# Performance work log

Hardware: AMD Instinct MI355X
Metric: run time of the kernel (lower is better)

## Reference

```python
import jax, jax.numpy as jnp
import numpy as np

N = 2060          # drug-graph nodes (m_drug_d_num)
F_OUT = 901       # out_feats, forced by Linear(901*2, ...)
M = 901 + (N - 1183)  # 1778 fused node rows
E = N * 64
N_TRAIN, N_TEST = 100000, 30000
EPS = 1e-5


def setup_inputs() -> dict:
    key = jax.random.key(0)
    ks = jax.random.split(key, 30)
    f32 = jnp.float32
    inp = {
        'x_feat': jax.random.normal(ks[0], (N, N), f32),
        'mirna_feat': jax.random.normal(ks[1], (M, F_OUT), f32),
        'Wg': jax.random.normal(ks[2], (N, F_OUT), f32) * 0.02,
        'att_src': jax.random.normal(ks[3], (F_OUT,), f32) * 0.05,
        'att_dst': jax.random.normal(ks[4], (F_OUT,), f32) * 0.05,
        'gat_b': jnp.zeros((F_OUT,), f32),
        'lw1': jax.random.normal(ks[5], (1, 2), f32) * 0.5,
        'lb1': jnp.zeros((1,), f32),
        'lw2': jax.random.normal(ks[6], (2, 1), f32) * 0.5,
        'lb2': jnp.zeros((2,), f32),
        'gw1': jax.random.normal(ks[7], (1, 2), f32) * 0.5,
        'gb1': jnp.zeros((1,), f32),
        'gw2': jax.random.normal(ks[8], (2, 1), f32) * 0.5,
        'gb2': jnp.zeros((2,), f32),
        'W1': jax.random.normal(ks[9], (2 * F_OUT, 1024), f32) * 0.02,
        'b1': jnp.zeros((1024,), f32),
        'W2': jax.random.normal(ks[10], (1024, 512), f32) * 0.03,
        'b2': jnp.zeros((512,), f32),
        'W3': jax.random.normal(ks[11], (512, 64), f32) * 0.04,
        'b3': jnp.zeros((64,), f32),
        'W4': jax.random.normal(ks[12], (64, 1), f32) * 0.1,
        'b4': jnp.zeros((1,), f32),
        'edge_index': jax.random.randint(ks[13], (2, E), 0, N, jnp.int32),
        'train_sample': jax.random.randint(ks[14], (N_TRAIN, 2), 0, M, jnp.int32),
        'test_sample': jax.random.randint(ks[15], (N_TEST, 2), 0, M, jnp.int32),
    }
    return inp


def _bn(x, axes):
    # BatchNorm in train mode (fresh module: gamma=1, beta=0, biased batch var)
    mu = x.mean(axes, keepdims=True)
    var = x.var(axes, keepdims=True)
    return (x - mu) * jax.lax.rsqrt(var + EPS)


def _gat(x, Wg, att_src, att_dst, gat_b, edge_index):
    # single-head PyG-style GATConv with self loops, negative_slope=0.2
    h = x @ Wg                                         # [N, F]
    loop = jnp.arange(N, dtype=edge_index.dtype)
    src = jnp.concatenate([edge_index[0], loop])
    dst = jnp.concatenate([edge_index[1], loop])
    a_s = h @ att_src                                  # [N]
    a_d = h @ att_dst
    e = jax.nn.leaky_relu(a_s[src] + a_d[dst], 0.2)    # per-edge logits
    emax = jax.ops.segment_max(e, dst, num_segments=N)
    ex = jnp.exp(e - emax[dst])
    denom = jax.ops.segment_sum(ex, dst, num_segments=N)
    alpha = ex / denom[dst]
    out = jax.ops.segment_sum(alpha[:, None] * h[src], dst, num_segments=N) + gat_b
    return jax.nn.relu(out)                            # F.relu in MGL (MGC relu is idempotent)


def _forward(x_feat, mirna_feat, Wg, att_src, att_dst, gat_b,
             lw1, lb1, lw2, lb2, gw1, gb1, gw2, gb2,
             W1, b1, W2, b2, W3, b3, W4, b4,
             edge_index, train_sample, test_sample):
    g = _gat(x_feat, Wg, att_src, att_dst, gat_b, edge_index)      # [N, 901]
    drug_view = jnp.concatenate([g[:901], g[1183:]], axis=0)       # [M, 901]
    x = jnp.stack([drug_view, mirna_feat], axis=1)                 # [M, 2, 901]  (B=M, C=2, H=1 dropped, W=901)

    # MS_CAM (channels=2, r=2), BN in train mode
    xl = jnp.einsum('mcw,oc->mow', x, lw1) + lb1[None, :, None]    # [M, 1, 901]
    xl = jax.nn.relu(_bn(xl, (0, 2)))
    xl = jnp.einsum('mcw,oc->mow', xl, lw2) + lb2[None, :, None]   # [M, 2, 901]
    xl = _bn(xl, (0, 2))

    gp = x.mean(axis=2)                                            # [M, 2] global avg pool
    xg = gp @ gw1.T + gb1                                          # [M, 1]
    xg = jax.nn.relu(_bn(xg, (0,)))
    xg = xg @ gw2.T + gb2                                          # [M, 2]
    xg = _bn(xg, (0,))

    wei = jax.nn.sigmoid(xl + xg[:, :, None])
    x = x * wei                                                    # [M, 2, 901]
    fused = (x[:, 0, :] + x[:, 1, :]) * 0.5                        # [M, 901]

    def score(pairs):
        emb = jnp.concatenate([fused[pairs[:, 0]], fused[pairs[:, 1]]], axis=1)  # [B, 1802]
        h = emb @ W1 + b1
        h = h @ W2 + b2
        h = h @ W3 + b3
        return jax.nn.sigmoid(h @ W4 + b4)

    return score(train_sample), score(test_sample)


def reference(x_feat, mirna_feat, Wg, att_src, att_dst, gat_b,
              lw1, lb1, lw2, lb2, gw1, gb1, gw2, gb2,
              W1, b1, W2, b2, W3, b3, W4, b4,
              edge_index, train_sample, test_sample):
    return _forward(x_feat, mirna_feat, Wg, att_src, att_dst, gat_b,
                    lw1, lb1, lw2, lb2, gw1, gb1, gw2, gb2,
                    W1, b1, W2, b2, W3, b3, W4, b4,
                    edge_index, train_sample, test_sample)
```

## Files before the change

kernel.cpp:

```cpp
#include <hip/hip_runtime.h>

typedef unsigned short u16;
typedef unsigned int   u32;

#define NN   2060
#define FF   901
#define HP   904
#define MM   1778
#define EE   131840
#define ETOT 133900
#define NTR  100000
#define NOUT 130000
#define MP   2112
#define KP   2080
#define NP   960
#define EPSV 1e-5f
#define NTOT 1601978.0

typedef __attribute__((ext_vector_type(4))) float f32x4;
typedef __attribute__((ext_vector_type(8))) short bf16x8;

#define GLL16(g,l) __builtin_amdgcn_global_load_lds( \
    (const __attribute__((address_space(1))) u32*)(g), \
    (__attribute__((address_space(3))) u32*)(l), 16, 0, 0)

__device__ __forceinline__ float bf2f(u16 u){ return __uint_as_float(((u32)u)<<16); }
__device__ __forceinline__ u16 f2bf(float f){
  u32 b = __float_as_uint(f);
  return (u16)((b + 0x7fffu + ((b>>16)&1u)) >> 16);
}
__device__ __forceinline__ float ldf(const void* p, size_t i, int bf){
  return bf ? bf2f(((const u16*)p)[i]) : ((const float*)p)[i];
}
__device__ __forceinline__ u16 ldb(const void* p, size_t i, int bf){
  return bf ? ((const u16*)p)[i] : f2bf(((const float*)p)[i]);
}
__device__ __forceinline__ float waveSum(float v){
  #pragma unroll
  for (int o = 32; o; o >>= 1) v += __shfl_down(v, o);
  return v;
}
__device__ __forceinline__ int waveSumI(int v){
  #pragma unroll
  for (int o = 32; o; o >>= 1) v += __shfl_down(v, o);
  return v;
}
__device__ __forceinline__ int flagWave(const u32* __restrict__ x){
  int l = threadIdx.x & 63;
  u32 w0 = x[l], w1 = x[l + 64];
  int big = (((w0 >> 7)  & 0xFFu) >= 0xC0u) + (((w0 >> 23) & 0xFFu) >= 0xC0u)
          + (((w1 >> 7)  & 0xFFu) >= 0xC0u) + (((w1 >> 23) & 0xFFu) >= 0xC0u);
  big = waveSumI(big);
  return (__shfl(big, 0) >= 8) ? 0 : 1;
}

__global__ __launch_bounds__(256) void pad_k(const void* __restrict__ X, const void* __restrict__ Wg,
                                             u16* __restrict__ Ap, u16* __restrict__ BT, int* bfp){
  __shared__ u16 tt[32][33];
  int bf = flagWave((const u32*)X);
  int bx = blockIdx.x, by = blockIdx.y, tid = threadIdx.x;
  if (bx == 0 && by == 0 && tid == 0) *bfp = bf;
  if (by < MP){
    int col = bx * 256 + tid, row = by;
    if (col >= KP) return;
    u16 v = 0;
    if (row < NN && col < NN) v = ldb(X, (size_t)row * NN + col, bf);
    Ap[(size_t)row * KP + col] = v;
  } else {
    if (bx) return;
    int t = by - MP;
    int kb = (t % 65) * 32, nb = (t / 65) * 32;
    int tx = tid & 31, ty = tid >> 5;
    #pragma unroll
    for (int i = 0; i < 4; ++i){
      int k = kb + ty + 8*i, n = nb + tx;
      u16 v = 0;
      if (k < NN && n < FF) v = ldb(Wg, (size_t)k * FF + n, bf);
      tt[ty + 8*i][tx] = v;
    }
    __syncthreads();
    #pragma unroll
    for (int i = 0; i < 4; ++i){
      int n = nb + ty + 8*i, k = kb + tx;
      if (n < NP && k < KP) BT[(size_t)n * KP + k] = tt[tx][ty + 8*i];
    }
  }
}

__global__ __launch_bounds__(256) void gemm_k(const u16* __restrict__ A, const u16* __restrict__ BT,
                                              u16* __restrict__ h){
  __shared__ __align__(16) u16 sA[64*32];
  __shared__ __align__(16) u16 sB[64*32];
  int bm = blockIdx.x * 64, bn = blockIdx.y * 64;
  int tid = threadIdx.x, lane = tid & 63, wave = tid >> 6;
  int wm = (wave >> 1) * 32, wn = (wave & 1) * 32;
  f32x4 acc[2][2] = {};
  int srow = tid >> 2;
  int schunk = (tid & 3) ^ ((tid >> 3) & 3);
  const u16* gA = A  + (size_t)(bm + srow) * KP + schunk * 8;
  const u16* gB = BT + (size_t)(bn + srow) * KP + schunk * 8;
  u16* lA = sA + wave * 512;
  u16* lB = sB + wave * 512;
  int fr = lane & 15, quad = lane >> 4;
  int qs = quad ^ ((fr >> 1) & 3);
  const u16* pa0 = &sA[(wm      + fr) * 32 + qs * 8];
  const u16* pa1 = &sA[(wm + 16 + fr) * 32 + qs * 8];
  const u16* pb0 = &sB[(wn      + fr) * 32 + qs * 8];
  const u16* pb1 = &sB[(wn + 16 + fr) * 32 + qs * 8];
  const int KIT = KP / 32;
  for (int kt = 0; kt < KIT; ++kt){
    __syncthreads();
    GLL16(gA + kt * 32, lA);
    GLL16(gB + kt * 32, lB);
    __syncthreads();
    bf16x8 a0 = *(const bf16x8*)pa0;
    bf16x8 a1 = *(const bf16x8*)pa1;
    bf16x8 b0 = *(const bf16x8*)pb0;
    bf16x8 b1 = *(const bf16x8*)pb1;
    acc[0][0] = __builtin_amdgcn_mfma_f32_16x16x32_bf16(a0, b0, acc[0][0], 0,0,0);
    acc[0][1] = __builtin_amdgcn_mfma_f32_16x16x32_bf16(a0, b1, acc[0][1], 0,0,0);
    acc[1][0] = __builtin_amdgcn_mfma_f32_16x16x32_bf16(a1, b0, acc[1][0], 0,0,0);
    acc[1][1] = __builtin_amdgcn_mfma_f32_16x16x32_bf16(a1, b1, acc[1][1], 0,0,0);
  }
  #pragma unroll
  for (int im = 0; im < 2; ++im)
    #pragma unroll
    for (int in = 0; in < 2; ++in)
      #pragma unroll
      for (int i = 0; i < 4; ++i){
        int row = bm + wm + im*16 + quad*4 + i;
        int col = bn + wn + in*16 + fr;
        if (row < NN && col < FF) h[(size_t)row * HP + col] = f2bf(acc[im][in][i]);
      }
}

__global__ __launch_bounds__(64) void asd_k(const u16* __restrict__ h, const void* att_s, const void* att_d,
                                            float* a_s, float* a_d, const int* bfp){
  int bf = *bfp;
  int n = blockIdx.x, tid = threadIdx.x;
  float ss = 0, sd = 0;
  for (int f = tid; f < FF; f += 64){
    float hv = bf2f(h[(size_t)n * HP + f]);
    ss += hv * ldf(att_s, f, bf);
    sd += hv * ldf(att_d, f, bf);
  }
  ss = waveSum(ss); sd = waveSum(sd);
  if (tid == 0){ a_s[n] = ss; a_d[n] = sd; }
}

__global__ __launch_bounds__(256) void edge1_k(const int* __restrict__ ei, const float* __restrict__ a_s,
                                               const float* __restrict__ a_d, float* __restrict__ e_val,
                                               u32* __restrict__ emax, int* __restrict__ counts){
  int e = blockIdx.x * 256 + threadIdx.x;
  if (e >= ETOT) return;
  int src, dst;
  if (e < EE){ src = ei[e]; dst = ei[EE + e]; } else { src = dst = e - EE; }
  float x = a_s[src] + a_d[dst];
  float ev = x > 0.f ? x : 0.2f * x;
  e_val[e] = ev;
  u32 bits = __float_as_uint(ev);
  u32 enc = (bits & 0x80000000u) ? ~bits : (bits | 0x80000000u);
  atomicMax(&emax[dst], enc);
  atomicAdd(&counts[dst], 1);
}

__global__ __launch_bounds__(256) void scan_k(const int* __restrict__ counts, int* __restrict__ offs){
  __shared__ int part[256];
  int tid = threadIdx.x;
  const int CH = (NN + 255) / 256;
  int base = tid * CH, s = 0;
  for (int i = 0; i < CH; ++i){ int idx = base + i; if (idx < NN) s += counts[idx]; }
  part[tid] = s;
  __syncthreads();
  if (tid == 0){ int run = 0; for (int i = 0; i < 256; ++i){ int v = part[i]; part[i] = run; run += v; } }
  __syncthreads();
  int run = part[tid];
  for (int i = 0; i < CH; ++i){ int idx = base + i; if (idx < NN){ offs[idx] = run; run += counts[idx]; } }
  if (tid == 255) offs[NN] = run;
}

__global__ __launch_bounds__(256) void edge2_k(const int* __restrict__ ei, const float* __restrict__ e_val,
                                               const u32* __restrict__ emax, float* __restrict__ denom,
                                               const int* __restrict__ offs, int* __restrict__ fill,
                                               int* __restrict__ csr_src, float* __restrict__ csr_w){
  int e = blockIdx.x * 256 + threadIdx.x;
  if (e >= ETOT) return;
  int src, dst;
  if (e < EE){ src = ei[e]; dst = ei[EE + e]; } else { src = dst = e - EE; }
  u32 enc = emax[dst];
  u32 bits = (enc & 0x80000000u) ? (enc & 0x7fffffffu) : ~enc;
  float ex = expf(e_val[e] - __uint_as_float(bits));
  atomicAdd(&denom[dst], ex);
  int pos = offs[dst] + atomicAdd(&fill[dst], 1);
  csr_src[pos] = src; csr_w[pos] = ex;
}

__device__ __forceinline__ void acc8(float* a, uint4 v, float w){
  u32 arr[4] = {v.x, v.y, v.z, v.w};
  #pragma unroll
  for (int i = 0; i < 4; ++i){
    a[2*i]   += w * __uint_as_float((arr[i] & 0xFFFFu) << 16);
    a[2*i+1] += w * __uint_as_float(arr[i] & 0xFFFF0000u);
  }
}
__global__ __launch_bounds__(128) void aggr_k(const u16* __restrict__ h, const int* __restrict__ offs,
                                              const int* __restrict__ csr_src, const float* __restrict__ csr_w,
                                              const float* __restrict__ denom, const void* gat_b,
                                              float* __restrict__ g, const int* bfp){
  int bf = *bfp;
  int dst = blockIdx.x, tid = threadIdx.x;
  int o0 = offs[dst], o1 = offs[dst + 1];
  float inv = 1.0f / denom[dst];
  __shared__ int   sS[128];
  __shared__ float sW[128];
  const int c = tid;
  float a[8] = {0,0,0,0,0,0,0,0};
  for (int base = o0; base < o1; base += 128){
    int nb = min(128, o1 - base);
    __syncthreads();
    if (tid < nb){ sS[tid] = csr_src[base + tid]; sW[tid] = csr_w[base + tid] * inv; }
    __syncthreads();
    if (c < 113){
      int k = 0;
      for (; k + 4 <= nb; k += 4){
        int   i0 = sS[k], i1 = sS[k+1], i2 = sS[k+2], i3 = sS[k+3];
        float w0 = sW[k], w1 = sW[k+1], w2 = sW[k+2], w3 = sW[k+3];
        uint4 v0 = ((const uint4*)(h + (size_t)i0 * HP))[c];
        uint4 v1 = ((const uint4*)(h + (size_t)i1 * HP))[c];
        uint4 v2 = ((const uint4*)(h + (size_t)i2 * HP))[c];
        uint4 v3 = ((const uint4*)(h + (size_t)i3 * HP))[c];
        acc8(a, v0, w0); acc8(a, v1, w1); acc8(a, v2, w2); acc8(a, v3, w3);
      }
      for (; k < nb; ++k){
        uint4 v0 = ((const uint4*)(h + (size_t)sS[k] * HP))[c];
        acc8(a, v0, sW[k]);
      }
    }
  }
  if (c < 113){
    int f0 = 8 * c;
    float r[8];
    #pragma unroll
    for (int i = 0; i < 8; ++i){
      float v = a[i] + ((f0 + i) < FF ? ldf(gat_b, f0 + i, bf) : 0.f);
      r[i] = v > 0.f ? v : 0.f;
    }
    float4* go = (float4*)(g + (size_t)dst * HP);
    go[2*c]   = make_float4(r[0], r[1], r[2], r[3]);
    go[2*c+1] = make_float4(r[4], r[5], r[6], r[7]);
  }
}

__global__ __launch_bounds__(256) void statsA_k(const float* __restrict__ g, const void* __restrict__ mirna,
                                                const void* lw1, const void* lb1,
                                                float* __restrict__ gp, float2* __restrict__ pA, const int* bfp){
  int bf = *bfp;
  int m = blockIdx.x, tid = threadIdx.x;
  int gr = m < 901 ? m : m + 282;
  float w00 = ldf(lw1,0,bf), w01 = ldf(lw1,1,bf), bb = ldf(lb1,0,bf);
  float sx0 = 0, sx1 = 0, sl = 0, sl2 = 0;
  for (int w = tid; w < FF; w += 256){
    float x0 = g[(size_t)gr * HP + w];
    float x1 = ldf(mirna, (size_t)m * FF + w, bf);
    sx0 += x0; sx1 += x1;
    float xl = w00*x0 + w01*x1 + bb;
    sl += xl; sl2 += xl*xl;
  }
  sx0 = waveSum(sx0); sx1 = waveSum(sx1); sl = waveSum(sl); sl2 = waveSum(sl2);
  __shared__ float sh[4][4];
  int wv = tid >> 6;
  if ((tid & 63) == 0){ sh[0][wv]=sx0; sh[1][wv]=sx1; sh[2][wv]=sl; sh[3][wv]=sl2; }
  __syncthreads();
  if (tid == 0){
    float t0 = sh[0][0]+sh[0][1]+sh[0][2]+sh[0][3];
    float t1 = sh[1][0]+sh[1][1]+sh[1][2]+sh[1][3];
    float t2 = sh[2][0]+sh[2][1]+sh[2][2]+sh[2][3];
    float t3 = sh[3][0]+sh[3][1]+sh[3][2]+sh[3][3];
    gp[2*m] = t0 / (float)FF; gp[2*m+1] = t1 / (float)FF;
    pA[m] = make_float2(t2, t3);
  }
}

__global__ __launch_bounds__(256) void xg_k(const float* __restrict__ gp, const void* gw1, const void* gb1,
                                            const void* gw2, float* __restrict__ xg2b,
                                            const float2* __restrict__ pA, double* __restrict__ Sd,
                                            const int* bfp){
  int bf = *bfp;
  __shared__ float xs[MM];
  __shared__ float red[2][4];
  __shared__ float bc[3];
  int tid = threadIdx.x;
  float s = 0, s2 = 0;
  for (int m = tid; m < MM; m += 256){ float2 p = pA[m]; s += p.x; s2 += p.y; }
  s = waveSum(s); s2 = waveSum(s2);
  if ((tid & 63) == 0){ red[0][tid>>6] = s; red[1][tid>>6] = s2; }
  __syncthreads();
  if (tid == 0){
    Sd[0] = (double)(red[0][0]+red[0][1]+red[0][2]+red[0][3]);
    Sd[1] = (double)(red[1][0]+red[1][1]+red[1][2]+red[1][3]);
  }
  __syncthreads();
  float g10 = ldf(gw1,0,bf), g11 = ldf(gw1,1,bf), b1v = ldf(gb1,0,bf);
  s = 0; s2 = 0;
  for (int m = tid; m < MM; m += 256){
    float v = g10*gp[2*m] + g11*gp[2*m+1] + b1v;
    xs[m] = v; s += v; s2 += v*v;
  }
  s = waveSum(s); s2 = waveSum(s2);
  __syncthreads();
  if ((tid & 63) == 0){ red[0][tid>>6] = s; red[1][tid>>6] = s2; }
  __syncthreads();
  if (tid == 0){
    float t  = red[0][0]+red[0][1]+red[0][2]+red[0][3];
    float t2 = red[1][0]+red[1][1]+red[1][2]+red[1][3];
    float mean = t / (float)MM, var = t2 / (float)MM - mean*mean;
    bc[0] = mean; bc[1] = rsqrtf(var + EPSV);
  }
  __syncthreads();
  float mean = bc[0], rs = bc[1];
  s = 0; s2 = 0;
  for (int m = tid; m < MM; m += 256){
    float r = (xs[m] - mean) * rs; r = r > 0.f ? r : 0.f;
    xs[m] = r; s += r; s2 += r*r;
  }
  s = waveSum(s); s2 = waveSum(s2);
  __syncthreads();
  if ((tid & 63) == 0){ red[0][tid>>6] = s; red[1][tid>>6] = s2; }
  __syncthreads();
  if (tid == 0){
    float t  = red[0][0]+red[0][1]+red[0][2]+red[0][3];
    float t2 = red[1][0]+red[1][1]+red[1][2]+red[1][3];
    float mrg = t / (float)MM, vrg = t2 / (float)MM - mrg*mrg;
    float g20 = ldf(gw2,0,bf), g21 = ldf(gw2,1,bf);
    bc[0] = mrg;
    bc[1] = g20 * rsqrtf(g20*g20*vrg + EPSV);
    bc[2] = g21 * rsqrtf(g21*g21*vrg + EPSV);
  }
  __syncthreads();
  float mrg = bc[0], c0 = bc[1], c1 = bc[2];
  for (int m = tid; m < MM; m += 256){
    float d = xs[m] - mrg;
    xg2b[2*m] = c0 * d; xg2b[2*m+1] = c1 * d;
  }
}

__global__ __launch_bounds__(256) void statsB_k(const float* __restrict__ g, const void* __restrict__ mirna,
                                                const void* lw1, const void* lb1,
                                                const double* __restrict__ S, float2* __restrict__ pB,
                                                const int* bfp){
  int bf = *bfp;
  int m = blockIdx.x, tid = threadIdx.x;
  int gr = m < 901 ? m : m + 282;
  float w00 = ldf(lw1,0,bf), w01 = ldf(lw1,1,bf), bb = ldf(lb1,0,bf);
  float mu1 = (float)(S[0] / NTOT);
  float rs1 = rsqrtf((float)(S[1] / NTOT) - mu1*mu1 + EPSV);
  float sr = 0, sr2 = 0;
  for (int w = tid; w < FF; w += 256){
    float x0 = g[(size_t)gr * HP + w];
    float x1 = ldf(mirna, (size_t)m * FF + w, bf);
    float xl = w00*x0 + w01*x1 + bb;
    float r = (xl - mu1) * rs1; r = r > 0.f ? r : 0.f;
    sr += r; sr2 += r*r;
  }
  sr = waveSum(sr); sr2 = waveSum(sr2);
  __shared__ float sh[2][4];
  if ((tid & 63) == 0){ sh[0][tid>>6] = sr; sh[1][tid>>6] = sr2; }
  __syncthreads();
  if (tid == 0) pB[m] = make_float2(sh[0][0]+sh[0][1]+sh[0][2]+sh[0][3],
                                    sh[1][0]+sh[1][1]+sh[1][2]+sh[1][3]);
}

__global__ __launch_bounds__(256) void redB_k(const float2* __restrict__ pB, double* __restrict__ Sd){
  int tid = threadIdx.x;
  float s = 0, s2 = 0;
  for (int m = tid; m < MM; m += 256){ float2 p = pB[m]; s += p.x; s2 += p.y; }
  s = waveSum(s); s2 = waveSum(s2);
  __shared__ float sh[2][4];
  if ((tid & 63) == 0){ sh[0][tid>>6] = s; sh[1][tid>>6] = s2; }
  __syncthreads();
  if (tid == 0){
    Sd[2] = (double)(sh[0][0]+sh[0][1]+sh[0][2]+sh[0][3]);
    Sd[3] = (double)(sh[1][0]+sh[1][1]+sh[1][2]+sh[1][3]);
  }
}

__global__ __launch_bounds__(256) void fs_k(const float* __restrict__ g, const void* __restrict__ mirna,
                                            const void* lw1, const void* lb1, const void* lw2,
                                            const double* __restrict__ S, const float* __restrict__ xg2b,
                                            const float* __restrict__ u1,
                                            float* __restrict__ s0, float* __restrict__ s1, const int* bfp){
  int bf = *bfp;
  int m = blockIdx.x, tid = threadIdx.x;
  int gr = m < 901 ? m : m + 282;
  float w00 = ldf(lw1,0,bf), w01 = ldf(lw1,1,bf), bb = ldf(lb1,0,bf);
  float mu1 = (float)(S[0] / NTOT);
  float rs1 = rsqrtf((float)(S[1] / NTOT) - mu1*mu1 + EPSV);
  float mr  = (float)(S[2] / NTOT);
  float vr  = (float)(S[3] / NTOT) - mr*mr;
  float l20 = ldf(lw2,0,bf), l21 = ldf(lw2,1,bf);
  float A0 = l20 * rsqrtf(l20*l20*vr + EPSV);
  float A1 = l21 * rsqrtf(l21*l21*vr + EPSV);
  float xa = xg2b[2*m], xb = xg2b[2*m+1];
  float p0 = 0, p1 = 0;
  for (int w = tid; w < FF; w += 256){
    float x0 = g[(size_t)gr * HP + w];
    float x1 = ldf(mirna, (size_t)m * FF + w, bf);
    float xl = w00*x0 + w01*x1 + bb;
    float r = (xl - mu1) * rs1; r = r > 0.f ? r : 0.f;
    float rc = r - mr;
    float z0 = A0*rc + xa, z1 = A1*rc + xb;
    float sg0 = 1.f / (1.f + expf(-z0));
    float sg1 = 1.f / (1.f + expf(-z1));
    float f = 0.5f * (x0*sg0 + x1*sg1);
    p0 += f * u1[w]; p1 += f * u1[901 + w];
  }
  p0 = waveSum(p0); p1 = waveSum(p1);
  __shared__ float sh[2][4];
  if ((tid & 63) == 0){ sh[0][tid>>6] = p0; sh[1][tid>>6] = p1; }
  __syncthreads();
  if (tid == 0){
    s0[m] = sh[0][0]+sh[0][1]+sh[0][2]+sh[0][3];
    s1[m] = sh[1][0]+sh[1][1]+sh[1][2]+sh[1][3];
  }
}

__global__ __launch_bounds__(64) void coll1_k(const void* __restrict__ W3, const void* __restrict__ W4,
                                              const void* b3, const void* b4, float* __restrict__ u3,
                                              double* cacc, const int* bfp){
  int bf = *bfp;
  int ob = blockIdx.x, tid = threadIdx.x;
  float s = (ob < 512) ? ldf(W3, ob*64 + tid, bf) * ldf(W4, tid, bf)
                       : ldf(b3, tid, bf) * ldf(W4, tid, bf);
  s = waveSum(s);
  if (tid == 0){
    if (ob < 512) u3[ob] = s;
    else atomicAdd(cacc, (double)(s + ldf(b4, 0, bf)));
  }
}
__global__ __launch_bounds__(256) void coll2_k(const void* __restrict__ W2, const void* __restrict__ b2,
                                               const float* __restrict__ u3, float* __restrict__ u2,
                                               double* cacc, const int* bfp){
  int bf = *bfp;
  int ob = blockIdx.x, tid = threadIdx.x;
  float s = 0;
  if (ob < 1024){
    for (int j = tid; j < 512; j += 256) s += ldf(W2, (size_t)ob * 512 + j, bf) * u3[j];
  } else {
    for (int j = tid; j < 512; j += 256) s += ldf(b2, j, bf) * u3[j];
  }
  s = waveSum(s);
  __shared__ float sh[4];
  if ((tid & 63) == 0) sh[tid>>6] = s;
  __syncthreads();
  if (tid == 0){
    float t = sh[0]+sh[1]+sh[2]+sh[3];
    if (ob < 1024) u2[ob] = t; else atomicAdd(cacc, (double)t);
  }
}
__global__ __launch_bounds__(256) void coll3_k(const void* __restrict__ W1, const void* __restrict__ b1,
                                               const float* __restrict__ u2, float* __restrict__ u1,
                                               double* cacc, const int* bfp){
  int bf = *bfp;
  int ob = blockIdx.x, tid = threadIdx.x;
  float s = 0;
  if (ob < 1802){
    for (int j = tid; j < 1024; j += 256) s += ldf(W1, (size_t)ob * 1024 + j, bf) * u2[j];
  } else {
    for (int j = tid; j < 1024; j += 256) s += ldf(b1, j, bf) * u2[j];
  }
  s = waveSum(s);
  __shared__ float sh[4];
  if ((tid & 63) == 0) sh[tid>>6] = s;
  __syncthreads();
  if (tid == 0){
    float t = sh[0]+sh[1]+sh[2]+sh[3];
    if (ob < 1802) u1[ob] = t; else atomicAdd(cacc, (double)t);
  }
}

__global__ __launch_bounds__(256) void out_k(const int* __restrict__ tr, const int* __restrict__ te,
                                             const float* __restrict__ s0, const float* __restrict__ s1,
                                             const double* __restrict__ cacc, void* __restrict__ out,
                                             const int* bfp){
  int bf = *bfp;
  int b = blockIdx.x * 256 + threadIdx.x;
  if (b >= NOUT) return;
  int i, j;
  if (b < NTR){ i = tr[2*b]; j = tr[2*b + 1]; }
  else { int t = b - NTR; i = te[2*t]; j = te[2*t + 1]; }
  float z = s0[i] + s1[j] + (float)cacc[0];
  float v = 1.f / (1.f + expf(-z));
  if (bf) ((u16*)out)[b] = f2bf(v);
  else    ((float*)out)[b] = v;
}

extern "C" void kernel_launch(void* const* d_in, const int* in_sizes, int n_in,
                              void* d_out, int out_size, void* d_ws, size_t ws_size,
                              hipStream_t stream){
  const void* x_feat = d_in[0];
  const void* mirna  = d_in[1];
  const void* Wg     = d_in[2];
  const void* att_s  = d_in[3];
  const void* att_d  = d_in[4];
  const void* gat_b  = d_in[5];
  const void* lw1    = d_in[6];
  const void* lb1    = d_in[7];
  const void* lw2    = d_in[8];
  const void* gw1    = d_in[10];
  const void* gb1    = d_in[11];
  const void* gw2    = d_in[12];
  const void* W1     = d_in[14];
  const void* b1     = d_in[15];
  const void* W2     = d_in[16];
  const void* b2     = d_in[17];
  const void* W3     = d_in[18];
  const void* b3     = d_in[19];
  const void* W4     = d_in[20];
  const void* b4     = d_in[21];
  const int* ei      = (const int*)d_in[22];
  const int* tr      = (const int*)d_in[23];
  const int* te      = (const int*)d_in[24];

  char* ws = (char*)d_ws;
  size_t off = 0;
  auto alloc = [&](size_t bytes)->size_t{ size_t o = off; off += (bytes + 255) & ~(size_t)255; return o; };
  size_t oA  = alloc((size_t)MP*KP*2);
  size_t oBT = alloc((size_t)NP*KP*2);
  size_t oH  = alloc((size_t)NN*HP*2);
  size_t oEV = alloc((size_t)ETOT*4);
  size_t oCS = alloc((size_t)ETOT*4);
  size_t oCW = alloc((size_t)ETOT*4);
  size_t oAS = alloc(NN*4);
  size_t oAD = alloc(NN*4);
  size_t oOF = alloc((NN+1)*4);
  size_t oGP = alloc(MM*2*4);
  size_t oXG = alloc(MM*2*4);
  size_t oS0 = alloc(MM*4);
  size_t oS1 = alloc(MM*4);
  size_t oU3 = alloc(512*4);
  size_t oU2 = alloc(1024*4);
  size_t oU1 = alloc(1802*4);
  size_t oPA = alloc(MM*8);
  size_t oPB = alloc(MM*8);
  size_t oSS = alloc(4*8);
  size_t oBF = alloc(4);
  size_t zstart = off;
  size_t oC  = alloc(8);
  size_t oMX = alloc(NN*4);
  size_t oDN = alloc(NN*4);
  size_t oCT = alloc(NN*4);
  size_t oFL = alloc(NN*4);
  size_t zend = off;

  u16*   Ap   = (u16*)(ws+oA);
  u16*   BT   = (u16*)(ws+oBT);
  u16*   h    = (u16*)(ws+oH);
  float* gbuf = (float*)(ws+oA);
  float* e_val= (float*)(ws+oEV);
  int*   csrS = (int*)(ws+oCS);
  float* csrW = (float*)(ws+oCW);
  float* a_s  = (float*)(ws+oAS);
  float* a_d  = (float*)(ws+oAD);
  int*   offs = (int*)(ws+oOF);
  float* gp   = (float*)(ws+oGP);
  float* xg2b = (float*)(ws+oXG);
  float* s0   = (float*)(ws+oS0);
  float* s1   = (float*)(ws+oS1);
  float* u3   = (float*)(ws+oU3);
  float* u2   = (float*)(ws+oU2);
  float* u1   = (float*)(ws+oU1);
  float2* pA  = (float2*)(ws+oPA);
  float2* pB  = (float2*)(ws+oPB);
  double* Sd  = (double*)(ws+oSS);
  int*   bfp  = (int*)(ws+oBF);
  double* cacc= (double*)(ws+oC);
  u32*   emax = (u32*)(ws+oMX);
  float* denom= (float*)(ws+oDN);
  int*   cnts = (int*)(ws+oCT);
  int*   fill = (int*)(ws+oFL);

  hipMemsetAsync(ws + zstart, 0, zend - zstart, stream);

  pad_k  <<<dim3(9, MP + 65*30), 256, 0, stream>>>(x_feat, Wg, Ap, BT, bfp);
  coll1_k<<<513,  64,  0, stream>>>(W3, W4, b3, b4, u3, cacc, bfp);
  coll2_k<<<1025, 256, 0, stream>>>(W2, b2, u3, u2, cacc, bfp);
  coll3_k<<<1803, 256, 0, stream>>>(W1, b1, u2, u1, cacc, bfp);
  gemm_k <<<dim3(MP/64, NP/64), 256, 0, stream>>>(Ap, BT, h);
  asd_k  <<<NN, 64, 0, stream>>>(h, att_s, att_d, a_s, a_d, bfp);
  edge1_k<<<(ETOT+255)/256, 256, 0, stream>>>(ei, a_s, a_d, e_val, emax, cnts);
  scan_k <<<1, 256, 0, stream>>>(cnts, offs);
  edge2_k<<<(ETOT+255)/256, 256, 0, stream>>>(ei, e_val, emax, denom, offs, fill, csrS, csrW);
  aggr_k <<<NN, 128, 0, stream>>>(h, offs, csrS, csrW, denom, gat_b, gbuf, bfp);
  statsA_k<<<MM, 256, 0, stream>>>(gbuf, mirna, lw1, lb1, gp, pA, bfp);
  xg_k   <<<1, 256, 0, stream>>>(gp, gw1, gb1, gw2, xg2b, pA, Sd, bfp);
  statsB_k<<<MM, 256, 0, stream>>>(gbuf, mirna, lw1, lb1, Sd, pB, bfp);
  redB_k <<<1, 256, 0, stream>>>(pB, Sd);
  fs_k   <<<MM, 256, 0, stream>>>(gbuf, mirna, lw1, lb1, lw2, Sd, xg2b, u1, s0, s1, bfp);
  out_k  <<<(NOUT+255)/256, 256, 0, stream>>>(tr, te, s0, s1, cacc, d_out, bfp);
}
```

Before: 286.6 us.

## Fuse weight-collapse, zeroing and stats kernels into neighbouring GAT kernels

Folds the memset and the W3/W4 collapse into the padding kernel, folds the W1 collapse into edge1, and fuses the per-row statsA reduction into the aggregation kernel. Aggregation now only runs the node rows actually consumed. Edge scores are recomputed in edge2 instead of being stored, and the double atomic constant accumulator is replaced by three plain floats. This cuts kernel launches and memory traffic at the cost of heavier, more heterogeneous kernels.

```diff
diff --git a/kernel.cpp b/kernel.cpp
--- a/kernel.cpp
+++ b/kernel.cpp
@@ -55,7 +55,13 @@
 }
 
 __global__ __launch_bounds__(256) void pad_k(const void* __restrict__ X, const void* __restrict__ Wg,
-                                             u16* __restrict__ Ap, u16* __restrict__ BT, int* bfp){
+                                             const void* __restrict__ W3, const void* __restrict__ W4,
+                                             const void* __restrict__ b3, const void* __restrict__ b4,
+                                             u16* __restrict__ Ap, u16* __restrict__ BT,
+                                             float* __restrict__ u3, float* __restrict__ cp,
+                                             u32* __restrict__ emax, int* __restrict__ cnts,
+                                             int* __restrict__ fill, float* __restrict__ denom,
+                                             int* bfp){
   __shared__ u16 tt[32][33];
   int bf = flagWave((const u32*)X);
   int bx = blockIdx.x, by = blockIdx.y, tid = threadIdx.x;
@@ -66,7 +72,7 @@
     u16 v = 0;
     if (row < NN && col < NN) v = ldb(X, (size_t)row * NN + col, bf);
     Ap[(size_t)row * KP + col] = v;
-  } else {
+  } else if (by < MP + 1950){
     if (bx) return;
     int t = by - MP;
     int kb = (t % 65) * 32, nb = (t / 65) * 32;
@@ -84,6 +90,16 @@
       int n = nb + ty + 8*i, k = kb + tx;
       if (n < NP && k < KP) BT[(size_t)n * KP + k] = tt[tx][ty + 8*i];
     }
+  } else if (by == MP + 1950){
+    if (bx) return;
+    for (int i = tid; i < NN; i += 256){ emax[i] = 0u; cnts[i] = 0; fill[i] = 0; denom[i] = 0.f; }
+  } else {
+    if (bx || tid >= 64) return;
+    int ob = by - (MP + 1951);
+    float s = (ob < 512) ? ldf(W3, (size_t)ob*64 + tid, bf) * ldf(W4, tid, bf)
+                         : ldf(b3, tid, bf) * ldf(W4, tid, bf);
+    s = waveSum(s);
+    if (tid == 0){ if (ob < 512) u3[ob] = s; else cp[0] = s + ldf(b4, 0, bf); }
   }
 }
 
@@ -134,6 +150,27 @@
       }
 }
 
+__global__ __launch_bounds__(256) void coll2_k(const void* __restrict__ W2, const void* __restrict__ b2,
+                                               const float* __restrict__ u3, float* __restrict__ u2,
+                                               float* __restrict__ cp, const int* bfp){
+  int bf = *bfp;
+  int ob = blockIdx.x, tid = threadIdx.x;
+  float s = 0;
+  if (ob < 1024){
+    for (int j = tid; j < 512; j += 256) s += ldf(W2, (size_t)ob * 512 + j, bf) * u3[j];
+  } else {
+    for (int j = tid; j < 512; j += 256) s += ldf(b2, j, bf) * u3[j];
+  }
+  s = waveSum(s);
+  __shared__ float sh[4];
+  if ((tid & 63) == 0) sh[tid>>6] = s;
+  __syncthreads();
+  if (tid == 0){
+    float t = sh[0]+sh[1]+sh[2]+sh[3];
+    if (ob < 1024) u2[ob] = t; else cp[1] = t;
+  }
+}
+
 __global__ __launch_bounds__(64) void asd_k(const u16* __restrict__ h, const void* att_s, const void* att_d,
                                             float* a_s, float* a_d, const int* bfp){
   int bf = *bfp;
@@ -149,19 +186,40 @@
 }
 
 __global__ __launch_bounds__(256) void edge1_k(const int* __restrict__ ei, const float* __restrict__ a_s,
-                                               const float* __restrict__ a_d, float* __restrict__ e_val,
-                                               u32* __restrict__ emax, int* __restrict__ counts){
-  int e = blockIdx.x * 256 + threadIdx.x;
-  if (e >= ETOT) return;
-  int src, dst;
-  if (e < EE){ src = ei[e]; dst = ei[EE + e]; } else { src = dst = e - EE; }
-  float x = a_s[src] + a_d[dst];
-  float ev = x > 0.f ? x : 0.2f * x;
-  e_val[e] = ev;
-  u32 bits = __float_as_uint(ev);
-  u32 enc = (bits & 0x80000000u) ? ~bits : (bits | 0x80000000u);
-  atomicMax(&emax[dst], enc);
-  atomicAdd(&counts[dst], 1);
+                                               const float* __restrict__ a_d,
+                                               u32* __restrict__ emax, int* __restrict__ counts,
+                                               const void* __restrict__ W1, const void* __restrict__ b1,
+                                               const float* __restrict__ u2, float* __restrict__ u1,
+                                               float* __restrict__ cp, const int* bfp){
+  int blk = blockIdx.x, tid = threadIdx.x, bf = *bfp;
+  int e = blk * 256 + tid;
+  if (e < ETOT){
+    int src, dst;
+    if (e < EE){ src = ei[e]; dst = ei[EE + e]; } else { src = dst = e - EE; }
+    float x = a_s[src] + a_d[dst];
+    float ev = x > 0.f ? x : 0.2f * x;
+    u32 bits = __float_as_uint(ev);
+    u32 enc = (bits & 0x80000000u) ? ~bits : (bits | 0x80000000u);
+    atomicMax(&emax[dst], enc);
+    atomicAdd(&counts[dst], 1);
+  }
+  if (blk < 451){
+    __shared__ float sh[4];
+    #pragma unroll 1
+    for (int r = 0; r < 4; ++r){
+      int ob = blk * 4 + r;
+      if (ob <= 1802){
+        float s = 0;
+        if (ob < 1802){ for (int j = tid; j < 1024; j += 256) s += ldf(W1, (size_t)ob*1024 + j, bf) * u2[j]; }
+        else          { for (int j = tid; j < 1024; j += 256) s += ldf(b1, j, bf) * u2[j]; }
+        s = waveSum(s);
+        __syncthreads();
+        if ((tid & 63) == 0) sh[tid >> 6] = s;
+        __syncthreads();
+        if (tid == 0){ float t = sh[0]+sh[1]+sh[2]+sh[3]; if (ob < 1802) u1[ob] = t; else cp[2] = t; }
+      }
+    }
+  }
 }
 
 __global__ __launch_bounds__(256) void scan_k(const int* __restrict__ counts, int* __restrict__ offs){
@@ -179,7 +237,8 @@
   if (tid == 255) offs[NN] = run;
 }
 
-__global__ __launch_bounds__(256) void edge2_k(const int* __restrict__ ei, const float* __restrict__ e_val,
+__global__ __launch_bounds__(256) void edge2_k(const int* __restrict__ ei, const float* __restrict__ a_s,
+                                               const float* __restrict__ a_d,
                                                const u32* __restrict__ emax, float* __restrict__ denom,
                                                const int* __restrict__ offs, int* __restrict__ fill,
                                                int* __restrict__ csr_src, float* __restrict__ csr_w){
@@ -187,9 +246,11 @@
   if (e >= ETOT) return;
   int src, dst;
   if (e < EE){ src = ei[e]; dst = ei[EE + e]; } else { src = dst = e - EE; }
+  float x = a_s[src] + a_d[dst];
+  float ev = x > 0.f ? x : 0.2f * x;
   u32 enc = emax[dst];
   u32 bits = (enc & 0x80000000u) ? (enc & 0x7fffffffu) : ~enc;
-  float ex = expf(e_val[e] - __uint_as_float(bits));
+  float ex = expf(ev - __uint_as_float(bits));
   atomicAdd(&denom[dst], ex);
   int pos = offs[dst] + atomicAdd(&fill[dst], 1);
   csr_src[pos] = src; csr_w[pos] = ex;
@@ -206,13 +267,18 @@
 __global__ __launch_bounds__(128) void aggr_k(const u16* __restrict__ h, const int* __restrict__ offs,
                                               const int* __restrict__ csr_src, const float* __restrict__ csr_w,
                                               const float* __restrict__ denom, const void* gat_b,
-                                              float* __restrict__ g, const int* bfp){
-  int bf = *bfp;
-  int dst = blockIdx.x, tid = threadIdx.x;
+                                              const void* __restrict__ mirna,
+                                              const void* lw1, const void* lb1,
+                                              float* __restrict__ g, float* __restrict__ gp,
+                                              float2* __restrict__ pA, const int* bfp){
+  int bf = *bfp;
+  int m = blockIdx.x, tid = threadIdx.x;
+  int dst = m < 901 ? m : m + 282;
   int o0 = offs[dst], o1 = offs[dst + 1];
   float inv = 1.0f / denom[dst];
   __shared__ int   sS[128];
   __shared__ float sW[128];
+  __shared__ float red[4][2];
   const int c = tid;
   float a[8] = {0,0,0,0,0,0,0,0};
   for (int base = o0; base < o1; base += 128){
@@ -237,47 +303,35 @@
       }
     }
   }
+  float w00 = ldf(lw1,0,bf), w01 = ldf(lw1,1,bf), bb = ldf(lb1,0,bf);
+  float sx0 = 0, sx1 = 0, sl = 0, sl2 = 0;
   if (c < 113){
     int f0 = 8 * c;
     float r[8];
     #pragma unroll
     for (int i = 0; i < 8; ++i){
-      float v = a[i] + ((f0 + i) < FF ? ldf(gat_b, f0 + i, bf) : 0.f);
-      r[i] = v > 0.f ? v : 0.f;
+      bool inb = (f0 + i) < FF;
+      float v = a[i] + (inb ? ldf(gat_b, f0 + i, bf) : 0.f);
+      v = v > 0.f ? v : 0.f;
+      r[i] = inb ? v : 0.f;
+      if (inb){
+        float x1 = ldf(mirna, (size_t)m * FF + f0 + i, bf);
+        float xl = w00*r[i] + w01*x1 + bb;
+        sx0 += r[i]; sx1 += x1; sl += xl; sl2 += xl*xl;
+      }
     }
     float4* go = (float4*)(g + (size_t)dst * HP);
     go[2*c]   = make_float4(r[0], r[1], r[2], r[3]);
     go[2*c+1] = make_float4(r[4], r[5], r[6], r[7]);
   }
-}
-
-__global__ __launch_bounds__(256) void statsA_k(const float* __restrict__ g, const void* __restrict__ mirna,
-                                                const void* lw1, const void* lb1,
-                                                float* __restrict__ gp, float2* __restrict__ pA, const int* bfp){
-  int bf = *bfp;
-  int m = blockIdx.x, tid = threadIdx.x;
-  int gr = m < 901 ? m : m + 282;
-  float w00 = ldf(lw1,0,bf), w01 = ldf(lw1,1,bf), bb = ldf(lb1,0,bf);
-  float sx0 = 0, sx1 = 0, sl = 0, sl2 = 0;
-  for (int w = tid; w < FF; w += 256){
-    float x0 = g[(size_t)gr * HP + w];
-    float x1 = ldf(mirna, (size_t)m * FF + w, bf);
-    sx0 += x0; sx1 += x1;
-    float xl = w00*x0 + w01*x1 + bb;
-    sl += xl; sl2 += xl*xl;
-  }
   sx0 = waveSum(sx0); sx1 = waveSum(sx1); sl = waveSum(sl); sl2 = waveSum(sl2);
-  __shared__ float sh[4][4];
   int wv = tid >> 6;
-  if ((tid & 63) == 0){ sh[0][wv]=sx0; sh[1][wv]=sx1; sh[2][wv]=sl; sh[3][wv]=sl2; }
-  __syncthreads();
-  if (tid == 0){
-    float t0 = sh[0][0]+sh[0][1]+sh[0][2]+sh[0][3];
-    float t1 = sh[1][0]+sh[1][1]+sh[1][2]+sh[1][3];
-    float t2 = sh[2][0]+sh[2][1]+sh[2][2]+sh[2][3];
-    float t3 = sh[3][0]+sh[3][1]+sh[3][2]+sh[3][3];
-    gp[2*m] = t0 / (float)FF; gp[2*m+1] = t1 / (float)FF;
-    pA[m] = make_float2(t2, t3);
+  if ((tid & 63) == 0){ red[0][wv]=sx0; red[1][wv]=sx1; red[2][wv]=sl; red[3][wv]=sl2; }
+  __syncthreads();
+  if (tid == 0){
+    gp[2*m]   = (red[0][0]+red[0][1]) / (float)FF;
+    gp[2*m+1] = (red[1][0]+red[1][1]) / (float)FF;
+    pA[m] = make_float2(red[2][0]+red[2][1], red[3][0]+red[3][1]);
   }
 }
 
@@ -424,63 +478,9 @@
   }
 }
 
-__global__ __launch_bounds__(64) void coll1_k(const void* __restrict__ W3, const void* __restrict__ W4,
-                                              const void* b3, const void* b4, float* __restrict__ u3,
-                                              double* cacc, const int* bfp){
-  int bf = *bfp;
-  int ob = blockIdx.x, tid = threadIdx.x;
-  float s = (ob < 512) ? ldf(W3, ob*64 + tid, bf) * ldf(W4, tid, bf)
-                       : ldf(b3, tid, bf) * ldf(W4, tid, bf);
-  s = waveSum(s);
-  if (tid == 0){
-    if (ob < 512) u3[ob] = s;
-    else atomicAdd(cacc, (double)(s + ldf(b4, 0, bf)));
-  }
-}
-__global__ __launch_bounds__(256) void coll2_k(const void* __restrict__ W2, const void* __restrict__ b2,
-                                               const float* __restrict__ u3, float* __restrict__ u2,
-                                               double* cacc, const int* bfp){
-  int bf = *bfp;
-  int ob = blockIdx.x, tid = threadIdx.x;
-  float s = 0;
-  if (ob < 1024){
-    for (int j = tid; j < 512; j += 256) s += ldf(W2, (size_t)ob * 512 + j, bf) * u3[j];
-  } else {
-    for (int j = tid; j < 512; j += 256) s += ldf(b2, j, bf) * u3[j];
-  }
-  s = waveSum(s);
-  __shared__ float sh[4];
-  if ((tid & 63) == 0) sh[tid>>6] = s;
-  __syncthreads();
-  if (tid == 0){
-    float t = sh[0]+sh[1]+sh[2]+sh[3];
-    if (ob < 1024) u2[ob] = t; else atomicAdd(cacc, (double)t);
-  }
-}
-__global__ __launch_bounds__(256) void coll3_k(const void* __restrict__ W1, const void* __restrict__ b1,
-                                               const float* __restrict__ u2, float* __restrict__ u1,
-                                               double* cacc, const int* bfp){
-  int bf = *bfp;
-  int ob = blockIdx.x, tid = threadIdx.x;
-  float s = 0;
-  if (ob < 1802){
-    for (int j = tid; j < 1024; j += 256) s += ldf(W1, (size_t)ob * 1024 + j, bf) * u2[j];
-  } else {
-    for (int j = tid; j < 1024; j += 256) s += ldf(b1, j, bf) * u2[j];
-  }
-  s = waveSum(s);
-  __shared__ float sh[4];
-  if ((tid & 63) == 0) sh[tid>>6] = s;
-  __syncthreads();
-  if (tid == 0){
-    float t = sh[0]+sh[1]+sh[2]+sh[3];
-    if (ob < 1802) u1[ob] = t; else atomicAdd(cacc, (double)t);
-  }
-}
-
 __global__ __launch_bounds__(256) void out_k(const int* __restrict__ tr, const int* __restrict__ te,
                                              const float* __restrict__ s0, const float* __restrict__ s1,
-                                             const double* __restrict__ cacc, void* __restrict__ out,
+                                             const float* __restrict__ cp, void* __restrict__ out,
                                              const int* bfp){
   int bf = *bfp;
   int b = blockIdx.x * 256 + threadIdx.x;
@@ -488,7 +488,7 @@
   int i, j;
   if (b < NTR){ i = tr[2*b]; j = tr[2*b + 1]; }
   else { int t = b - NTR; i = te[2*t]; j = te[2*t + 1]; }
-  float z = s0[i] + s1[j] + (float)cacc[0];
+  float z = s0[i] + s1[j] + cp[0] + cp[1] + cp[2];
   float v = 1.f / (1.f + expf(-z));
   if (bf) ((u16*)out)[b] = f2bf(v);
   else    ((float*)out)[b] = v;
@@ -527,7 +527,6 @@
   size_t oA  = alloc((size_t)MP*KP*2);
   size_t oBT = alloc((size_t)NP*KP*2);
   size_t oH  = alloc((size_t)NN*HP*2);
-  size_t oEV = alloc((size_t)ETOT*4);
   size_t oCS = alloc((size_t)ETOT*4);
   size_t oCW = alloc((size_t)ETOT*4);
   size_t oAS = alloc(NN*4);
@@ -543,20 +542,17 @@
   size_t oPA = alloc(MM*8);
   size_t oPB = alloc(MM*8);
   size_t oSS = alloc(4*8);
+  size_t oCP = alloc(3*4);
   size_t oBF = alloc(4);
-  size_t zstart = off;
-  size_t oC  = alloc(8);
   size_t oMX = alloc(NN*4);
   size_t oDN = alloc(NN*4);
   size_t oCT = alloc(NN*4);
   size_t oFL = alloc(NN*4);
-  size_t zend = off;
 
   u16*   Ap   = (u16*)(ws+oA);
   u16*   BT   = (u16*)(ws+oBT);
   u16*   h    = (u16*)(ws+oH);
   float* gbuf = (float*)(ws+oA);
-  float* e_val= (float*)(ws+oEV);
   int*   csrS = (int*)(ws+oCS);
   float* csrW = (float*)(ws+oCW);
   float* a_s  = (float*)(ws+oAS);
@@ -572,29 +568,25 @@
   float2* pA  = (float2*)(ws+oPA);
   float2* pB  = (float2*)(ws+oPB);
   double* Sd  = (double*)(ws+oSS);
+  float* cp   = (float*)(ws+oCP);
   int*   bfp  = (int*)(ws+oBF);
-  double* cacc= (double*)(ws+oC);
   u32*   emax = (u32*)(ws+oMX);
   float* denom= (float*)(ws+oDN);
   int*   cnts = (int*)(ws+oCT);
   int*   fill = (int*)(ws+oFL);
 
-  hipMemsetAsync(ws + zstart, 0, zend - zstart, stream);
-
-  pad_k  <<<dim3(9, MP + 65*30), 256, 0, stream>>>(x_feat, Wg, Ap, BT, bfp);
-  coll1_k<<<513,  64,  0, stream>>>(W3, W4, b3, b4, u3, cacc, bfp);
-  coll2_k<<<1025, 256, 0, stream>>>(W2, b2, u3, u2, cacc, bfp);
-  coll3_k<<<1803, 256, 0, stream>>>(W1, b1, u2, u1, cacc, bfp);
+  pad_k  <<<dim3(9, MP + 1950 + 1 + 513), 256, 0, stream>>>(
+      x_feat, Wg, W3, W4, b3, b4, Ap, BT, u3, cp, emax, cnts, fill, denom, bfp);
   gemm_k <<<dim3(MP/64, NP/64), 256, 0, stream>>>(Ap, BT, h);
+  coll2_k<<<1025, 256, 0, stream>>>(W2, b2, u3, u2, cp, bfp);
   asd_k  <<<NN, 64, 0, stream>>>(h, att_s, att_d, a_s, a_d, bfp);
-  edge1_k<<<(ETOT+255)/256, 256, 0, stream>>>(ei, a_s, a_d, e_val, emax, cnts);
+  edge1_k<<<(ETOT+255)/256, 256, 0, stream>>>(ei, a_s, a_d, emax, cnts, W1, b1, u2, u1, cp, bfp);
   scan_k <<<1, 256, 0, stream>>>(cnts, offs);
-  edge2_k<<<(ETOT+255)/256, 256, 0, stream>>>(ei, e_val, emax, denom, offs, fill, csrS, csrW);
-  aggr_k <<<NN, 128, 0, stream>>>(h, offs, csrS, csrW, denom, gat_b, gbuf, bfp);
-  statsA_k<<<MM, 256, 0, stream>>>(gbuf, mirna, lw1, lb1, gp, pA, bfp);
+  edge2_k<<<(ETOT+255)/256, 256, 0, stream>>>(ei, a_s, a_d, emax, denom, offs, fill, csrS, csrW);
+  aggr_k <<<MM, 128, 0, stream>>>(h, offs, csrS, csrW, denom, gat_b, mirna, lw1, lb1, gbuf, gp, pA, bfp);
   xg_k   <<<1, 256, 0, stream>>>(gp, gw1, gb1, gw2, xg2b, pA, Sd, bfp);
   statsB_k<<<MM, 256, 0, stream>>>(gbuf, mirna, lw1, lb1, Sd, pB, bfp);
   redB_k <<<1, 256, 0, stream>>>(pB, Sd);
   fs_k   <<<MM, 256, 0, stream>>>(gbuf, mirna, lw1, lb1, lw2, Sd, xg2b, u1, s0, s1, bfp);
-  out_k  <<<(NOUT+255)/256, 256, 0, stream>>>(tr, te, s0, s1, cacc, d_out, bfp);
-}
+  out_k  <<<(NOUT+255)/256, 256, 0, stream>>>(tr, te, s0, s1, cp, d_out, bfp);
+}
```

New measurement: 284.3 us. About the same (-0.8%).
